# Kernel tuning notes

Measured on AMD Instinct MI355X. Metric: run time of the kernel, lower is better.

The kernel has to match this reference:

```python
import jax, jax.numpy as jnp
import numpy as np

EPS = 0.01          # layer_norm_epsilon from Gpt2Config
ROPE_THETA = 10000.0


def _rms_norm(x, w, eps=EPS):
    # RmsNorm over the last (head_size) axis, computed in fp32
    var = jnp.mean(jnp.square(x.astype(jnp.float32)), axis=-1, keepdims=True)
    return (x.astype(jnp.float32) * jax.lax.rsqrt(var + eps)).astype(x.dtype) * w


def _rope_cos_sin(seq_len, head_size, dtype):
    # default (NeoX/llama-style) rotary embeddings over the full head dim
    inv_freq = 1.0 / (ROPE_THETA ** (jnp.arange(0, head_size, 2, dtype=jnp.float32) / head_size))
    ang = jnp.arange(seq_len, dtype=jnp.float32)[:, None] * inv_freq[None, :]   # [S, D/2]
    cos = jnp.concatenate([jnp.cos(ang), jnp.cos(ang)], axis=-1).astype(dtype)  # [S, D]
    sin = jnp.concatenate([jnp.sin(ang), jnp.sin(ang)], axis=-1).astype(dtype)
    return cos, sin


def _rotate_half(x):
    half = x.shape[-1] // 2
    return jnp.concatenate([-x[..., half:], x[..., :half]], axis=-1)


def _apply_rope(x, cos, sin):
    # x: [B, S, H, D]; cos/sin: [S, D]
    return x * cos[None, :, None, :] + _rotate_half(x) * sin[None, :, None, :]


def setup_inputs() -> dict:
    key = jax.random.key(0)
    ks = jax.random.split(key, 3)
    B, S, E, H, D = 4, 2048, 2048, 16, 128
    x = jax.random.normal(ks[0], (B, S, E), dtype=jnp.float32)
    w_qkv = jax.random.normal(ks[1], (E, 3, H, D), dtype=jnp.float32) * 0.02
    w_proj = jax.random.normal(ks[2], (H, D, E), dtype=jnp.float32) * 0.02
    q_norm_w = jnp.ones((D,), dtype=jnp.float32)
    k_norm_w = jnp.ones((D,), dtype=jnp.float32)
    return {"x": x, "w_qkv": w_qkv, "w_proj": w_proj,
            "q_norm_w": q_norm_w, "k_norm_w": k_norm_w}


def reference(x, w_qkv, w_proj, q_norm_w, k_norm_w):
    B, S, E = x.shape
    _, _, H, D = w_qkv.shape

    # fused QKV projection (no bias)
    qkv = jnp.einsum('bse,ekhd->kbshd', x, w_qkv)  # [3, B, S, H, D]
    q, k, v = qkv[0], qkv[1], qkv[2]

    # qk RmsNorm over head_size
    q = _rms_norm(q, q_norm_w)
    k = _rms_norm(k, k_norm_w)

    # rotary embeddings
    cos, sin = _rope_cos_sin(S, D, x.dtype)
    q = _apply_rope(q, cos, sin)
    k = _apply_rope(k, cos, sin)

    # scaled dot-product attention, upcast to fp32, causal mask
    scale = 1.0 / jnp.sqrt(jnp.float32(D))
    scores = jnp.einsum('bshd,bthd->bhst', q.astype(jnp.float32),
                        k.astype(jnp.float32)) * scale        # [B, H, S, S]
    causal = jnp.arange(S)[:, None] >= jnp.arange(S)[None, :]  # [S, S]
    scores = jnp.where(causal[None, None], scores, jnp.float32(-1e9))
    attn = jax.nn.softmax(scores, axis=-1).astype(x.dtype)

    out = jnp.einsum('bhst,bthd->bshd', attn, v)               # [B, S, H, D]
    y = jnp.einsum('bshd,hde->bse', out, w_proj)               # output projection
    return y
```

## Files before the change

### kernel.cpp

```cpp
#include <hip/hip_runtime.h>
#include <hip/hip_bf16.h>
#include <math.h>

typedef unsigned short u16;
typedef __attribute__((ext_vector_type(8))) short short8;
typedef __attribute__((ext_vector_type(4))) float f32x4;
typedef __attribute__((ext_vector_type(4))) unsigned short ushort4v;
typedef __attribute__((ext_vector_type(8))) unsigned short ushort8v;

#define DEV static __device__ __forceinline__

DEV u16 f2bf(float f) {
    unsigned int x = __builtin_bit_cast(unsigned int, f);
    x += 0x7fffu + ((x >> 16) & 1u);
    return (u16)(x >> 16);
}
DEV float bf2f(u16 u) {
    unsigned int x = ((unsigned int)u) << 16;
    return __builtin_bit_cast(float, x);
}
DEV unsigned int pk_bf_trunc(float lo, float hi) {
    return __builtin_amdgcn_perm(__builtin_bit_cast(unsigned int, hi),
                                 __builtin_bit_cast(unsigned int, lo), 0x07060302u);
}

DEV void gl_lds16(const u16* g, u16* l) {
    __builtin_amdgcn_global_load_lds(
        (const __attribute__((address_space(1))) void*)g,
        (__attribute__((address_space(3))) void*)l, 16, 0, 0);
}

DEV short8 ldsv(const u16* p) { return *(const short8*)p; }

__global__ __launch_bounds__(256) void k_x2bf(
    const float* __restrict__ in, u16* __restrict__ out)
{
    int idx = blockIdx.x * 256 + threadIdx.x;
    const float4* p = (const float4*)in + (size_t)idx * 2;
    float4 a = p[0], b = p[1];
    ushort8v v;
    v[0] = f2bf(a.x); v[1] = f2bf(a.y); v[2] = f2bf(a.z); v[3] = f2bf(a.w);
    v[4] = f2bf(b.x); v[5] = f2bf(b.y); v[6] = f2bf(b.z); v[7] = f2bf(b.w);
    *(ushort8v*)(out + (size_t)idx * 8) = v;
}

__global__ __launch_bounds__(256) void k_transpose_bf16(
    const float* __restrict__ in, u16* __restrict__ out, int R, int C)
{
    __shared__ u16 t[64][72];
    int r0 = blockIdx.y * 64, c0 = blockIdx.x * 64;
    int tid = threadIdx.x;
    for (int i = 0; i < 4; ++i) {
        int u = tid + i * 256;
        int r = u >> 4, c4 = (u & 15) * 4;
        const float4 v = *(const float4*)(in + (size_t)(r0 + r) * C + c0 + c4);
        t[c4 + 0][r] = f2bf(v.x); t[c4 + 1][r] = f2bf(v.y);
        t[c4 + 2][r] = f2bf(v.z); t[c4 + 3][r] = f2bf(v.w);
    }
    __syncthreads();
    for (int i = 0; i < 4; ++i) {
        int u = tid + i * 256;
        int c = u >> 4, r4 = (u & 15) * 4;
        ushort4v v;
        v[0] = t[c][r4]; v[1] = t[c][r4 + 1]; v[2] = t[c][r4 + 2]; v[3] = t[c][r4 + 3];
        *(ushort4v*)(out + (size_t)(c0 + c) * R + r0 + r4) = v;
    }
}

template <int MODE>
__global__ __launch_bounds__(512, 2) void k_gemm256(
    const u16* __restrict__ A, const u16* __restrict__ Bt,
    u16* __restrict__ outQ, u16* __restrict__ outK, u16* __restrict__ outV,
    float* __restrict__ outF, int M, int N, int K)
{
    __shared__ u16 sA[2][2][128 * 64];
    __shared__ u16 sB[2][2][128 * 64];
    const int tid = threadIdx.x;
    const int lane = tid & 63, wid = tid >> 6;
    const int wm = wid >> 2, wn = wid & 3;
    const int lm = lane & 15, lq = lane >> 4;
    const int row0 = blockIdx.y * 256, col0 = blockIdx.x * 256;

    const int rl = lane >> 3;
    const int clog = (lane & 7) ^ rl;
    const u16* gA = A  + (size_t)(row0 + rl) * K + clog * 8;
    const u16* gB = Bt + (size_t)(col0 + rl) * K + clog * 8;
    const int rg = wid * 16;

    auto stA = [&](int bb, int h, int kt) {
        const u16* g = gA + (size_t)(h * 128 + rg) * K + (size_t)kt * 64;
        u16* l = &sA[bb][h][rg * 64];
        gl_lds16(g, l);
        gl_lds16(g + (size_t)8 * K, l + 512);
    };
    auto stB = [&](int bb, int h, int kt) {
        const u16* g = gB + (size_t)(h * 128 + rg) * K + (size_t)kt * 64;
        u16* l = &sB[bb][h][rg * 64];
        gl_lds16(g, l);
        gl_lds16(g + (size_t)8 * K, l + 512);
    };

    const int sw  = lm & 7;
    const int axr = lm * 64;
    const int bxr = ((wn & 1) * 64 + lm) * 64;
    const int co0 = ((lq ^ sw) << 3);
    const int co1 = (((lq | 4) ^ sw) << 3);

    f32x4 acc[8][4];
#pragma unroll
    for (int a = 0; a < 8; ++a)
#pragma unroll
        for (int b = 0; b < 4; ++b) acc[a][b] = (f32x4){0.f, 0.f, 0.f, 0.f};

    short8 af[4][2], bf[4][2];
    const int NT = K >> 6;

    stB(0, 0, 0); stB(0, 1, 0); stA(0, 0, 0); stA(0, 1, 0);
    stB(1, 0, 1); stB(1, 1, 1);
    asm volatile("s_waitcnt vmcnt(4)" ::: "memory");
    __builtin_amdgcn_s_barrier();

    auto tile_step = [&](int T, int buf) {
        const u16* pA = &sA[buf][wm][0];
        const u16* pB = &sB[buf][wn >> 1][0];
        const int nb = buf ^ 1;
        const bool p1ok = (T + 1 < NT);
        const bool p2ok = (T + 2 < NT);

#pragma unroll
        for (int t = 0; t < 4; ++t) {
            af[t][0] = ldsv(pA + axr + t * 1024 + co0);
            af[t][1] = ldsv(pA + axr + t * 1024 + co1);
        }
#pragma unroll
        for (int j = 0; j < 2; ++j) {
            bf[j][0] = ldsv(pB + bxr + j * 1024 + co0);
            bf[j][1] = ldsv(pB + bxr + j * 1024 + co1);
        }
        if (p1ok) stA(nb, 0, T + 1);
        asm volatile("s_waitcnt lgkmcnt(8)" ::: "memory");
        __builtin_amdgcn_s_barrier();
        asm volatile("s_waitcnt lgkmcnt(0)" ::: "memory");
        __builtin_amdgcn_s_setprio(1);
#pragma unroll
        for (int t = 0; t < 4; ++t)
#pragma unroll
            for (int j = 0; j < 2; ++j)
#pragma unroll
                for (int kk = 0; kk < 2; ++kk)
                    acc[t][j] = __builtin_amdgcn_mfma_f32_16x16x32_bf16(
                        af[t][kk], bf[j][kk], acc[t][j], 0, 0, 0);
        __builtin_amdgcn_s_setprio(0);
        __builtin_amdgcn_s_barrier();

#pragma unroll
        for (int j = 0; j < 2; ++j) {
            bf[2 + j][0] = ldsv(pB + bxr + (2 + j) * 1024 + co0);
            bf[2 + j][1] = ldsv(pB + bxr + (2 + j) * 1024 + co1);
        }
        if (p1ok) stA(nb, 1, T + 1);
        __builtin_amdgcn_s_barrier();
        asm volatile("s_waitcnt lgkmcnt(0)" ::: "memory");
        __builtin_amdgcn_s_setprio(1);
#pragma unroll
        for (int t = 0; t < 4; ++t)
#pragma unroll
            for (int j = 0; j < 2; ++j)
#pragma unroll
                for (int kk = 0; kk < 2; ++kk)
                    acc[t][2 + j] = __builtin_amdgcn_mfma_f32_16x16x32_bf16(
                        af[t][kk], bf[2 + j][kk], acc[t][2 + j], 0, 0, 0);
        __builtin_amdgcn_s_setprio(0);
        __builtin_amdgcn_s_barrier();

#pragma unroll
        for (int t = 0; t < 4; ++t) {
            af[t][0] = ldsv(pA + axr + (4 + t) * 1024 + co0);
            af[t][1] = ldsv(pA + axr + (4 + t) * 1024 + co1);
        }
        if (p2ok) stB(buf, 0, T + 2);
        __builtin_amdgcn_s_barrier();
        asm volatile("s_waitcnt lgkmcnt(0)" ::: "memory");
        __builtin_amdgcn_s_setprio(1);
#pragma unroll
        for (int t = 0; t < 4; ++t)
#pragma unroll
            for (int j = 0; j < 2; ++j)
#pragma unroll
                for (int kk = 0; kk < 2; ++kk)
                    acc[4 + t][2 + j] = __builtin_amdgcn_mfma_f32_16x16x32_bf16(
                        af[t][kk], bf[2 + j][kk], acc[4 + t][2 + j], 0, 0, 0);
        __builtin_amdgcn_s_setprio(0);
        __builtin_amdgcn_s_barrier();

        if (p2ok) {
            stB(buf, 1, T + 2);
            asm volatile("s_waitcnt vmcnt(4)" ::: "memory");
        } else {
            asm volatile("s_waitcnt vmcnt(0)" ::: "memory");
        }
        __builtin_amdgcn_s_barrier();
        __builtin_amdgcn_s_setprio(1);
#pragma unroll
        for (int t = 0; t < 4; ++t)
#pragma unroll
            for (int j = 0; j < 2; ++j)
#pragma unroll
                for (int kk = 0; kk < 2; ++kk)
                    acc[4 + t][j] = __builtin_amdgcn_mfma_f32_16x16x32_bf16(
                        af[t][kk], bf[j][kk], acc[4 + t][j], 0, 0, 0);
        __builtin_amdgcn_s_setprio(0);
        __builtin_amdgcn_s_barrier();
    };

    for (int T = 0; T < NT; T += 2) {
        tile_step(T, 0);
        tile_step(T + 1, 1);
    }
    asm volatile("s_waitcnt vmcnt(0)" ::: "memory");

    if (MODE == 0) {
        int k3 = col0 >> 11;
        u16* dst = (k3 == 0) ? outQ : (k3 == 1) ? outK : outV;
#pragma unroll
        for (int it = 0; it < 8; ++it)
#pragma unroll
            for (int jt = 0; jt < 4; ++jt) {
                int c = col0 + wn * 64 + jt * 16 + lm;
                int hd = c & 2047, h = hd >> 7, d = hd & 127;
#pragma unroll
                for (int i = 0; i < 4; ++i) {
                    int r = row0 + wm * 128 + it * 16 + lq * 4 + i;
                    int b = r >> 11, s = r & 2047;
                    dst[((size_t)(b * 16 + h) * 2048 + s) * 128 + d] = f2bf(acc[it][jt][i]);
                }
            }
    } else {
#pragma unroll
        for (int it = 0; it < 8; ++it)
#pragma unroll
            for (int jt = 0; jt < 4; ++jt) {
                int c = col0 + wn * 64 + jt * 16 + lm;
#pragma unroll
                for (int i = 0; i < 4; ++i) {
                    int r = row0 + wm * 128 + it * 16 + lq * 4 + i;
                    outF[(size_t)r * N + c] = acc[it][jt][i];
                }
            }
    }
}

__global__ __launch_bounds__(256) void k_normrope(
    u16* __restrict__ X, const float* __restrict__ w, float oscale)
{
    int row = blockIdx.x * 4 + (threadIdx.x >> 6);
    int t = threadIdx.x & 63;
    int s = row & 2047;
    u16* p = X + (size_t)row * 128;
    float x0 = bf2f(p[t]), x1 = bf2f(p[t + 64]);
    float ss = x0 * x0 + x1 * x1;
    for (int m = 1; m < 64; m <<= 1) ss += __shfl_xor(ss, m);
    float r = rsqrtf(ss * (1.0f / 128.0f) + 0.01f);
    float a = x0 * r * w[t];
    float b = x1 * r * w[t + 64];
    float freq = exp2f(-13.287712379549449f * ((float)t * (1.0f / 64.0f)));
    float ang = (float)s * freq;
    float sn, c;
    sincosf(ang, &sn, &c);
    p[t]      = f2bf((a * c - b * sn) * oscale);
    p[t + 64] = f2bf((b * c + a * sn) * oscale);
}

__global__ __launch_bounds__(256) void k_vtrans(
    const u16* __restrict__ Vh, u16* __restrict__ Vt, int S)
{
    __shared__ u16 t[128][68];
    int bh = blockIdx.y, s0 = blockIdx.x * 64;
    int tid = threadIdx.x;
    const u16* src = Vh + ((size_t)bh * S + s0) * 128;
    for (int i = 0; i < 4; ++i) {
        int u = tid + i * 256;
        int r = u >> 4, c8 = (u & 15) * 8;
        ushort8v v = *(const ushort8v*)(src + (size_t)r * 128 + c8);
        for (int j = 0; j < 8; ++j) t[c8 + j][r] = v[j];
    }
    __syncthreads();
    u16* dst = Vt + (size_t)bh * 128 * S + s0;
    for (int i = 0; i < 8; ++i) {
        int u = tid + i * 256;
        int d = u >> 4, s4 = (u & 15) * 4;
        ushort4v v;
        v[0] = t[d][s4]; v[1] = t[d][s4 + 1]; v[2] = t[d][s4 + 2]; v[3] = t[d][s4 + 3];
        *(ushort4v*)(dst + (size_t)d * S + s4) = v;
    }
}

template <bool DIAG>
DEV void flash_core(int kb, int lq, int lm, int qcol,
                    const u16* __restrict__ sKf, const u16* __restrict__ sVf,
                    const short8 qf[4], f32x4 oacc[8],
                    float& mprev, float& lsum, u16* __restrict__ sPw,
                    f32x4 sacc[4])
{
    for (int nt = 0; nt < 4; ++nt) sacc[nt] = (f32x4){0.f, 0.f, 0.f, 0.f};
    for (int nt = 0; nt < 4; ++nt)
        for (int kc = 0; kc < 4; ++kc) {
            short8 kf = *(const short8*)(sKf + (nt * 16 + lm) * 128 +
                                         (((kc * 4 + lq) ^ lm) << 3));
            sacc[nt] = __builtin_amdgcn_mfma_f32_16x16x32_bf16(kf, qf[kc], sacc[nt], 0, 0, 0);
        }
}

DEV void flash_softmax_pv(int lq, int lm, int S_dummy,
                          const u16* __restrict__ sVf,
                          f32x4 oacc[8], float& mprev, float& lsum,
                          u16* __restrict__ sPw, f32x4 sacc[4])
{
    float mx = sacc[0][0];
    for (int nt = 0; nt < 4; ++nt)
        for (int i = 0; i < 4; ++i) mx = fmaxf(mx, sacc[nt][i]);
    mx = fmaxf(mx, __shfl_xor(mx, 16));
    mx = fmaxf(mx, __shfl_xor(mx, 32));
    float mnew = fmaxf(mprev, mx);
    float alpha = exp2f(mprev - mnew);
    float rs = 0.0f;
    for (int nt = 0; nt < 4; ++nt)
        for (int i = 0; i < 4; ++i) {
            float pv = exp2f(sacc[nt][i] - mnew);
            sacc[nt][i] = pv;
            rs += pv;
        }
    rs += __shfl_xor(rs, 16);
    rs += __shfl_xor(rs, 32);
    lsum = lsum * alpha + rs;
    mprev = mnew;

    for (int nt = 0; nt < 4; ++nt) {
        uint2 pk;
        pk.x = pk_bf_trunc(sacc[nt][0], sacc[nt][1]);
        pk.y = pk_bf_trunc(sacc[nt][2], sacc[nt][3]);
        *(uint2*)(sPw + lm * 64 +
                  ((((nt << 1) + (lq >> 1)) ^ (lm & 7)) << 3) + ((lq & 1) << 2)) = pk;
    }

    float alphar[4];
    for (int i = 0; i < 4; ++i) alphar[i] = __shfl(alpha, lq * 4 + i, 16);
    for (int f = 0; f < 8; ++f)
        for (int i = 0; i < 4; ++i) oacc[f][i] *= alphar[i];

    short8 pf[2];
    for (int kc = 0; kc < 2; ++kc)
        pf[kc] = *(const short8*)(sPw + lm * 64 + (((kc * 4 + lq) ^ (lm & 7)) << 3));
    for (int f = 0; f < 8; ++f)
        for (int kc = 0; kc < 2; ++kc) {
            short8 vf = *(const short8*)(sVf + (f * 16 + lm) * 64 +
                                         (((kc * 4 + lq) ^ (lm & 7)) << 3));
            oacc[f] = __builtin_amdgcn_mfma_f32_16x16x32_bf16(pf[kc], vf, oacc[f], 0, 0, 0);
        }
}

__global__ __launch_bounds__(256, 4) void k_flash(
    const u16* __restrict__ Qh, const u16* __restrict__ Kh,
    const u16* __restrict__ Vt, u16* __restrict__ ctx, int S)
{
    __shared__ u16 sK[64 * 128];
    __shared__ u16 sV[128 * 64];
    __shared__ u16 sP[4 * 16 * 64];
    int qi = 31 - (int)blockIdx.x;
    int bh = blockIdx.y;
    int b = bh >> 4, h = bh & 15;
    int tid = threadIdx.x, lane = tid & 63, w = tid >> 6;
    int lm = lane & 15, lq = lane >> 4;
    const u16* qbase = Qh + (size_t)bh * S * 128;
    u16* sPw = &sP[w * 16 * 64];

    int kck = lm ^ (w * 4 + lq);
    const u16* kg = Kh + (size_t)bh * S * 128 + (size_t)(w * 4 + lq) * 128 + kck * 8;
    int hi3 = lane >> 3, c3 = lane & 7;
    int vck = c3 ^ (hi3 & 7);
    const u16* vg = Vt + (size_t)bh * 128 * S + (size_t)(w * 8 + hi3) * S + vck * 8;

    auto stageK = [&](int kb) {
        const u16* g = kg + (size_t)kb * (64 * 128);
        for (int i = 0; i < 4; ++i)
            gl_lds16(g + i * (16 * 128), sK + (i * 16 + w * 4) * 128);
    };
    auto stageV = [&](int kb) {
        const u16* g = vg + kb * 64;
        for (int i = 0; i < 4; ++i)
            gl_lds16(g + (size_t)(i * 32) * S, sV + (i * 32 + w * 8) * 64);
    };

    int q0 = qi * 64 + w * 16;
    short8 qf[4];
    for (int kc = 0; kc < 4; ++kc)
        qf[kc] = *(const short8*)(qbase + (size_t)(q0 + lm) * 128 + kc * 32 + lq * 8);

    f32x4 oacc[8];
    for (int f = 0; f < 8; ++f) oacc[f] = (f32x4){0.f, 0.f, 0.f, 0.f};
    float mprev = -1e30f, lsum = 0.0f;
    int qcol = q0 + lm;

    stageK(0);
    stageV(0);
    __syncthreads();

    f32x4 sacc[4];
    for (int kb = 0; kb < qi; ++kb) {
        flash_core<false>(kb, lq, lm, qcol, sK, sV, qf, oacc, mprev, lsum, sPw, sacc);
        __syncthreads();
        stageK(kb + 1);
        flash_softmax_pv(lq, lm, S, sV, oacc, mprev, lsum, sPw, sacc);
        __syncthreads();
        stageV(kb + 1);
    }
    flash_core<true>(qi, lq, lm, qcol, sK, sV, qf, oacc, mprev, lsum, sPw, sacc);
    for (int nt = 0; nt < 4; ++nt)
        for (int i = 0; i < 4; ++i) {
            int kv = qi * 64 + nt * 16 + lq * 4 + i;
            if (kv > qcol) sacc[nt][i] = -1e30f;
        }
    __syncthreads();
    flash_softmax_pv(lq, lm, S, sV, oacc, mprev, lsum, sPw, sacc);

    float linv[4];
    for (int i = 0; i < 4; ++i)
        linv[i] = 1.0f / __shfl(lsum, lq * 4 + i, 16);
    u16* obase = ctx + (size_t)b * S * 2048 + h * 128;
    for (int f = 0; f < 8; ++f) {
        int d = f * 16 + lm;
        for (int i = 0; i < 4; ++i) {
            int s = qi * 64 + w * 16 + lq * 4 + i;
            obase[(size_t)s * 2048 + d] = f2bf(oacc[f][i] * linv[i]);
        }
    }
}

extern "C" void kernel_launch(void* const* d_in, const int* in_sizes, int n_in,
                              void* d_out, int out_size, void* d_ws, size_t ws_size,
                              hipStream_t stream)
{
    const float* x        = (const float*)d_in[0];
    const float* w_qkv    = (const float*)d_in[1];
    const float* w_proj   = (const float*)d_in[2];
    const float* q_norm_w = (const float*)d_in[3];
    const float* k_norm_w = (const float*)d_in[4];
    float* out = (float*)d_out;

    const int B = 4, S = 2048, E = 2048, H = 16;
    const int M  = B * S;
    const int N1 = 3 * E;
    const int N2 = E;
    const float QSCALE = 0.12751743f;

    char* ws = (char*)d_ws;
    size_t off = 0;
    auto alloc = [&](size_t bytes) {
        char* p = ws + off;
        off += (bytes + 255) & ~(size_t)255;
        return p;
    };
    u16* Wpt  = (u16*)alloc((size_t)E * E * 2);
    char* regR = alloc((size_t)M * N1 * 2);
    u16* Wqt  = (u16*)regR;
    u16* ctxp = (u16*)regR;
    u16* Qh = (u16*)alloc((size_t)M * E * 2);
    u16* Kh = (u16*)alloc((size_t)M * E * 2);
    u16* Vh = (u16*)alloc((size_t)M * E * 2);
    char* regV = alloc((size_t)M * E * 2);
    u16* xb = (u16*)regV;
    u16* Vt = (u16*)regV;

    k_x2bf<<<(M * E) / (256 * 8), 256, 0, stream>>>(x, xb);
    k_transpose_bf16<<<dim3(N1 / 64, E / 64), 256, 0, stream>>>(w_qkv, Wqt, E, N1);
    k_transpose_bf16<<<dim3(N2 / 64, E / 64), 256, 0, stream>>>(w_proj, Wpt, E, N2);
    k_gemm256<0><<<dim3(N1 / 256, M / 256), 512, 0, stream>>>(
        xb, Wqt, Qh, Kh, Vh, nullptr, M, N1, E);
    k_normrope<<<(B * H * S) / 4, 256, 0, stream>>>(Qh, q_norm_w, QSCALE);
    k_normrope<<<(B * H * S) / 4, 256, 0, stream>>>(Kh, k_norm_w, 1.0f);
    k_vtrans<<<dim3(S / 64, B * H), 256, 0, stream>>>(Vh, Vt, S);
    k_flash<<<dim3(32, B * H), 256, 0, stream>>>(Qh, Kh, Vt, ctxp, S);
    k_gemm256<1><<<dim3(N2 / 256, M / 256), 512, 0, stream>>>(
        ctxp, Wpt, nullptr, nullptr, nullptr, out, M, N2, E);
}
```

Baseline: 655.1 us.

## Process 32 query rows per wave in flash attention to reuse K/V fragments

The flash-attention kernel now has each wave handle two 16-row query sub-tiles, so a block covers 128 queries instead of 64. Each K and V fragment read from LDS feeds two MFMAs, halving LDS traffic and staging work per query. Causal masking moves into a lambda applied to the last two key tiles. The cost is double the accumulator registers, so launch bounds drop to 2 blocks per SM, and there are half as many blocks with coarser causal load imbalance.

Result: no change. 661.3 us (+0.9%).

```diff
diff --git a/kernel.cpp b/kernel.cpp
--- a/kernel.cpp
+++ b/kernel.cpp
@@ -295,84 +295,112 @@
     }
 }
 
-template <bool DIAG>
-DEV void flash_core(int kb, int lq, int lm, int qcol,
-                    const u16* __restrict__ sKf, const u16* __restrict__ sVf,
-                    const short8 qf[4], f32x4 oacc[8],
-                    float& mprev, float& lsum, u16* __restrict__ sPw,
-                    f32x4 sacc[4])
-{
-    for (int nt = 0; nt < 4; ++nt) sacc[nt] = (f32x4){0.f, 0.f, 0.f, 0.f};
+DEV void flash_core2(int lq, int lm, const u16* __restrict__ sKf,
+                     const short8 qf[4][2], f32x4 sacc[4][2])
+{
+#pragma unroll
     for (int nt = 0; nt < 4; ++nt)
+#pragma unroll
+        for (int c = 0; c < 2; ++c) sacc[nt][c] = (f32x4){0.f, 0.f, 0.f, 0.f};
+#pragma unroll
+    for (int nt = 0; nt < 4; ++nt)
+#pragma unroll
         for (int kc = 0; kc < 4; ++kc) {
-            short8 kf = *(const short8*)(sKf + (nt * 16 + lm) * 128 +
-                                         (((kc * 4 + lq) ^ lm) << 3));
-            sacc[nt] = __builtin_amdgcn_mfma_f32_16x16x32_bf16(kf, qf[kc], sacc[nt], 0, 0, 0);
-        }
-}
-
-DEV void flash_softmax_pv(int lq, int lm, int S_dummy,
-                          const u16* __restrict__ sVf,
-                          f32x4 oacc[8], float& mprev, float& lsum,
-                          u16* __restrict__ sPw, f32x4 sacc[4])
-{
-    float mx = sacc[0][0];
-    for (int nt = 0; nt < 4; ++nt)
-        for (int i = 0; i < 4; ++i) mx = fmaxf(mx, sacc[nt][i]);
-    mx = fmaxf(mx, __shfl_xor(mx, 16));
-    mx = fmaxf(mx, __shfl_xor(mx, 32));
-    float mnew = fmaxf(mprev, mx);
-    float alpha = exp2f(mprev - mnew);
-    float rs = 0.0f;
-    for (int nt = 0; nt < 4; ++nt)
-        for (int i = 0; i < 4; ++i) {
-            float pv = exp2f(sacc[nt][i] - mnew);
-            sacc[nt][i] = pv;
-            rs += pv;
-        }
-    rs += __shfl_xor(rs, 16);
-    rs += __shfl_xor(rs, 32);
-    lsum = lsum * alpha + rs;
-    mprev = mnew;
-
-    for (int nt = 0; nt < 4; ++nt) {
-        uint2 pk;
-        pk.x = pk_bf_trunc(sacc[nt][0], sacc[nt][1]);
-        pk.y = pk_bf_trunc(sacc[nt][2], sacc[nt][3]);
-        *(uint2*)(sPw + lm * 64 +
-                  ((((nt << 1) + (lq >> 1)) ^ (lm & 7)) << 3) + ((lq & 1) << 2)) = pk;
-    }
-
-    float alphar[4];
-    for (int i = 0; i < 4; ++i) alphar[i] = __shfl(alpha, lq * 4 + i, 16);
+            short8 kf = ldsv(sKf + (nt * 16 + lm) * 128 +
+                             (((kc * 4 + lq) ^ lm) << 3));
+#pragma unroll
+            for (int c = 0; c < 2; ++c)
+                sacc[nt][c] = __builtin_amdgcn_mfma_f32_16x16x32_bf16(
+                    kf, qf[kc][c], sacc[nt][c], 0, 0, 0);
+        }
+}
+
+DEV void flash_softmax_pv2(int lq, int lm, const u16* __restrict__ sVf,
+                           f32x4 oacc[8][2], float mprev[2], float lsum[2],
+                           u16* __restrict__ sPw, f32x4 sacc[4][2])
+{
+    float alpha[2];
+#pragma unroll
+    for (int c = 0; c < 2; ++c) {
+        float mx = sacc[0][c][0];
+#pragma unroll
+        for (int nt = 0; nt < 4; ++nt)
+#pragma unroll
+            for (int i = 0; i < 4; ++i) mx = fmaxf(mx, sacc[nt][c][i]);
+        mx = fmaxf(mx, __shfl_xor(mx, 16));
+        mx = fmaxf(mx, __shfl_xor(mx, 32));
+        float mnew = fmaxf(mprev[c], mx);
+        alpha[c] = exp2f(mprev[c] - mnew);
+        float rs = 0.0f;
+#pragma unroll
+        for (int nt = 0; nt < 4; ++nt)
+#pragma unroll
+            for (int i = 0; i < 4; ++i) {
+                float pv = exp2f(sacc[nt][c][i] - mnew);
+                sacc[nt][c][i] = pv;
+                rs += pv;
+            }
+        rs += __shfl_xor(rs, 16);
+        rs += __shfl_xor(rs, 32);
+        lsum[c] = lsum[c] * alpha[c] + rs;
+        mprev[c] = mnew;
+
+#pragma unroll
+        for (int nt = 0; nt < 4; ++nt) {
+            uint2 pk;
+            pk.x = pk_bf_trunc(sacc[nt][c][0], sacc[nt][c][1]);
+            pk.y = pk_bf_trunc(sacc[nt][c][2], sacc[nt][c][3]);
+            *(uint2*)(sPw + (c * 16 + lm) * 64 +
+                      ((((nt << 1) + (lq >> 1)) ^ (lm & 7)) << 3) + ((lq & 1) << 2)) = pk;
+        }
+    }
+
+    float alphar[2][4];
+#pragma unroll
+    for (int c = 0; c < 2; ++c)
+#pragma unroll
+        for (int i = 0; i < 4; ++i) alphar[c][i] = __shfl(alpha[c], lq * 4 + i, 16);
+#pragma unroll
     for (int f = 0; f < 8; ++f)
-        for (int i = 0; i < 4; ++i) oacc[f][i] *= alphar[i];
-
-    short8 pf[2];
+#pragma unroll
+        for (int c = 0; c < 2; ++c)
+#pragma unroll
+            for (int i = 0; i < 4; ++i) oacc[f][c][i] *= alphar[c][i];
+
+    short8 pf[2][2];
+#pragma unroll
     for (int kc = 0; kc < 2; ++kc)
-        pf[kc] = *(const short8*)(sPw + lm * 64 + (((kc * 4 + lq) ^ (lm & 7)) << 3));
+#pragma unroll
+        for (int c = 0; c < 2; ++c)
+            pf[kc][c] = ldsv(sPw + (c * 16 + lm) * 64 +
+                             (((kc * 4 + lq) ^ (lm & 7)) << 3));
+#pragma unroll
     for (int f = 0; f < 8; ++f)
+#pragma unroll
         for (int kc = 0; kc < 2; ++kc) {
-            short8 vf = *(const short8*)(sVf + (f * 16 + lm) * 64 +
-                                         (((kc * 4 + lq) ^ (lm & 7)) << 3));
-            oacc[f] = __builtin_amdgcn_mfma_f32_16x16x32_bf16(pf[kc], vf, oacc[f], 0, 0, 0);
-        }
-}
-
-__global__ __launch_bounds__(256, 4) void k_flash(
+            short8 vf = ldsv(sVf + (f * 16 + lm) * 64 +
+                             (((kc * 4 + lq) ^ (lm & 7)) << 3));
+#pragma unroll
+            for (int c = 0; c < 2; ++c)
+                oacc[f][c] = __builtin_amdgcn_mfma_f32_16x16x32_bf16(
+                    pf[kc][c], vf, oacc[f][c], 0, 0, 0);
+        }
+}
+
+__global__ __launch_bounds__(256, 2) void k_flash(
     const u16* __restrict__ Qh, const u16* __restrict__ Kh,
     const u16* __restrict__ Vt, u16* __restrict__ ctx, int S)
 {
     __shared__ u16 sK[64 * 128];
     __shared__ u16 sV[128 * 64];
-    __shared__ u16 sP[4 * 16 * 64];
-    int qi = 31 - (int)blockIdx.x;
+    __shared__ u16 sP[4 * 32 * 64];
+    int qi = 15 - (int)blockIdx.x;
     int bh = blockIdx.y;
     int b = bh >> 4, h = bh & 15;
     int tid = threadIdx.x, lane = tid & 63, w = tid >> 6;
     int lm = lane & 15, lq = lane >> 4;
     const u16* qbase = Qh + (size_t)bh * S * 128;
-    u16* sPw = &sP[w * 16 * 64];
+    u16* sPw = &sP[w * 32 * 64];
 
     int kck = lm ^ (w * 4 + lq);
     const u16* kg = Kh + (size_t)bh * S * 128 + (size_t)(w * 4 + lq) * 128 + kck * 8;
@@ -391,48 +419,71 @@
             gl_lds16(g + (size_t)(i * 32) * S, sV + (i * 32 + w * 8) * 64);
     };
 
-    int q0 = qi * 64 + w * 16;
-    short8 qf[4];
+    int qw0 = qi * 128 + w * 32;
+    short8 qf[4][2];
+#pragma unroll
     for (int kc = 0; kc < 4; ++kc)
-        qf[kc] = *(const short8*)(qbase + (size_t)(q0 + lm) * 128 + kc * 32 + lq * 8);
-
-    f32x4 oacc[8];
-    for (int f = 0; f < 8; ++f) oacc[f] = (f32x4){0.f, 0.f, 0.f, 0.f};
-    float mprev = -1e30f, lsum = 0.0f;
-    int qcol = q0 + lm;
+#pragma unroll
+        for (int c = 0; c < 2; ++c)
+            qf[kc][c] = *(const short8*)(qbase + (size_t)(qw0 + c * 16 + lm) * 128 +
+                                         kc * 32 + lq * 8);
+
+    f32x4 oacc[8][2];
+#pragma unroll
+    for (int f = 0; f < 8; ++f)
+#pragma unroll
+        for (int c = 0; c < 2; ++c) oacc[f][c] = (f32x4){0.f, 0.f, 0.f, 0.f};
+    float mprev[2] = {-1e30f, -1e30f}, lsum[2] = {0.0f, 0.0f};
 
     stageK(0);
     stageV(0);
     __syncthreads();
 
-    f32x4 sacc[4];
-    for (int kb = 0; kb < qi; ++kb) {
-        flash_core<false>(kb, lq, lm, qcol, sK, sV, qf, oacc, mprev, lsum, sPw, sacc);
+    f32x4 sacc[4][2];
+    auto mask_tile = [&](int kb) {
+#pragma unroll
+        for (int nt = 0; nt < 4; ++nt)
+#pragma unroll
+            for (int c = 0; c < 2; ++c)
+#pragma unroll
+                for (int i = 0; i < 4; ++i) {
+                    int kv = kb * 64 + nt * 16 + lq * 4 + i;
+                    if (kv > qw0 + c * 16 + lm) sacc[nt][c][i] = -1e30f;
+                }
+    };
+
+    int last = 2 * qi + 1;
+    for (int kb = 0; kb < last; ++kb) {
+        flash_core2(lq, lm, sK, qf, sacc);
+        if (kb == last - 1) mask_tile(kb);
         __syncthreads();
         stageK(kb + 1);
-        flash_softmax_pv(lq, lm, S, sV, oacc, mprev, lsum, sPw, sacc);
+        flash_softmax_pv2(lq, lm, sV, oacc, mprev, lsum, sPw, sacc);
         __syncthreads();
         stageV(kb + 1);
     }
-    flash_core<true>(qi, lq, lm, qcol, sK, sV, qf, oacc, mprev, lsum, sPw, sacc);
-    for (int nt = 0; nt < 4; ++nt)
-        for (int i = 0; i < 4; ++i) {
-            int kv = qi * 64 + nt * 16 + lq * 4 + i;
-            if (kv > qcol) sacc[nt][i] = -1e30f;
-        }
+    flash_core2(lq, lm, sK, qf, sacc);
+    mask_tile(last);
     __syncthreads();
-    flash_softmax_pv(lq, lm, S, sV, oacc, mprev, lsum, sPw, sacc);
-
-    float linv[4];
-    for (int i = 0; i < 4; ++i)
-        linv[i] = 1.0f / __shfl(lsum, lq * 4 + i, 16);
+    flash_softmax_pv2(lq, lm, sV, oacc, mprev, lsum, sPw, sacc);
+
+    float linv[2][4];
+#pragma unroll
+    for (int c = 0; c < 2; ++c)
+#pragma unroll
+        for (int i = 0; i < 4; ++i)
+            linv[c][i] = 1.0f / __shfl(lsum[c], lq * 4 + i, 16);
     u16* obase = ctx + (size_t)b * S * 2048 + h * 128;
+#pragma unroll
     for (int f = 0; f < 8; ++f) {
         int d = f * 16 + lm;
-        for (int i = 0; i < 4; ++i) {
-            int s = qi * 64 + w * 16 + lq * 4 + i;
-            obase[(size_t)s * 2048 + d] = f2bf(oacc[f][i] * linv[i]);
-        }
+#pragma unroll
+        for (int c = 0; c < 2; ++c)
+#pragma unroll
+            for (int i = 0; i < 4; ++i) {
+                int s = qw0 + c * 16 + lq * 4 + i;
+                obase[(size_t)s * 2048 + d] = f2bf(oacc[f][c][i] * linv[c][i]);
+            }
     }
 }
 
@@ -479,7 +530,7 @@
     k_normrope<<<(B * H * S) / 4, 256, 0, stream>>>(Qh, q_norm_w, QSCALE);
     k_normrope<<<(B * H * S) / 4, 256, 0, stream>>>(Kh, k_norm_w, 1.0f);
     k_vtrans<<<dim3(S / 64, B * H), 256, 0, stream>>>(Vh, Vt, S);
-    k_flash<<<dim3(32, B * H), 256, 0, stream>>>(Qh, Kh, Vt, ctxp, S);
+    k_flash<<<dim3(S / 128, B * H), 256, 0, stream>>>(Qh, Kh, Vt, ctxp, S);
     k_gemm256<1><<<dim3(N2 / 256, M / 256), 512, 0, stream>>>(
         ctxp, Wpt, nullptr, nullptr, nullptr, out, M, N2, E);
 }
```
